# Kernel optimization log

Hardware: AMD Instinct MI355X
Metric: run time of the kernel (lower is better)

## Reference

```python
import jax, jax.numpy as jnp
import numpy as np

D_MODEL = 256

def setup_inputs() -> dict:
    key = jax.random.key(0)
    ks = jax.random.split(key, 6)
    B, Tx, Tm, D = 4, 512, 512, D_MODEL
    s = 1.0 / np.sqrt(D)
    return {
        "x": jax.random.normal(ks[0], (B, Tx, D), jnp.float32),
        "memory": jax.random.normal(ks[1], (B, Tm, D), jnp.float32),
        "memory_mask": jnp.ones((B, Tm), jnp.int32),
        "ws1_w": jax.random.uniform(ks[2], (D, D), jnp.float32, -s, s),
        "ws1_b": jax.random.uniform(ks[3], (D,), jnp.float32, -s, s),
        "ws2_w": jax.random.uniform(ks[4], (D, D), jnp.float32, -s, s),
        "wst_w": jax.random.uniform(ks[5], (D,), jnp.float32, -s, s),
    }

def reference(x, memory, memory_mask, ws1_w, ws1_b, ws2_w, wst_w):
    # item1: [B,Tx,D], item2: [B,Tm,D]  (torch Linear: y = x @ W^T + b)
    item1 = jnp.einsum("bxd,ed->bxe", x, ws1_w) + ws1_b
    item2 = jnp.einsum("bmd,ed->bme", memory, ws2_w)
    # broadcast add -> [B,Tx,Tm,D], tanh, reduce by wst -> scores [B,Tx,Tm]
    item = jnp.tanh(item1[:, :, None, :] + item2[:, None, :, :])
    S = jnp.einsum("bxmd,d->bxm", item, wst_w)
    S = jnp.where(memory_mask[:, None, :] == 0, -jnp.inf, S)
    S = jax.nn.softmax(S, axis=-1)
    out = jnp.einsum("bxm,bmd->bxd", S, memory)
    return (out, S)
```

## Files before the change

### kernel.cpp

```cpp
#include <hip/hip_runtime.h>

#define D_MODEL 256
#define TX 512
#define TM 512

__device__ __forceinline__ float fexp2(float x) { return __builtin_amdgcn_exp2f(x); }
__device__ __forceinline__ float frcp(float x)  { return __builtin_amdgcn_rcpf(x); }

__device__ __forceinline__ float quad(float4 a, float4 e, float4 w, float acc) {
    float p1 = fmaf(a.x, e.x, 1.f);
    float p2 = fmaf(a.y, e.y, 1.f);
    float p3 = fmaf(a.z, e.z, 1.f);
    float p4 = fmaf(a.w, e.w, 1.f);
    float p12 = p1 * p2;
    float p34 = p3 * p4;
    float q12 = fmaf(w.x, p2, w.y * p1);
    float q34 = fmaf(w.z, p4, w.w * p3);
    float N   = fmaf(q12, p34, q34 * p12);
    float D   = p12 * p34;
    return fmaf(N, frcp(D), acc);
}

__global__ __launch_bounds__(256) void gemm_exp2(
    const float* __restrict__ x,   const float* __restrict__ mem,
    const float* __restrict__ w1,  const float* __restrict__ b1,
    const float* __restrict__ w2,
    float* __restrict__ E1, float* __restrict__ E2p)
{
    const float C_SCALE = 2.8853900817779268f;
    const float* A; const float* W;
    int r0, n0;
    if (blockIdx.z == 0) { A = x;  W = w1; r0 = blockIdx.x * 64; n0 = blockIdx.y * 64; }
    else                 { A = w2; W = mem; r0 = blockIdx.y * 64; n0 = blockIdx.x * 64; }

    __shared__ float As[2][16][68];
    __shared__ float Ws[2][16][68];
    const int tid = threadIdx.x;
    const int tx = tid & 15, ty = tid >> 4;
    const int rl = tid >> 2, g = tid & 3;
    float acc[4][4] = {};
    const float* Ap = A + (size_t)(r0 + rl) * 256 + g * 4;
    const float* Wp = W + (size_t)(n0 + rl) * 256 + g * 4;

    {
        float4 a4 = *(const float4*)Ap;
        float4 w4 = *(const float4*)Wp;
        As[0][g*4+0][rl] = a4.x; As[0][g*4+1][rl] = a4.y;
        As[0][g*4+2][rl] = a4.z; As[0][g*4+3][rl] = a4.w;
        Ws[0][g*4+0][rl] = w4.x; Ws[0][g*4+1][rl] = w4.y;
        Ws[0][g*4+2][rl] = w4.z; Ws[0][g*4+3][rl] = w4.w;
    }
    __syncthreads();

    for (int k0 = 0; k0 < 16; ++k0) {
        const int cur = k0 & 1;
        float4 an, wn;
        if (k0 < 15) {
            an = *(const float4*)(Ap + (k0 + 1) * 16);
            wn = *(const float4*)(Wp + (k0 + 1) * 16);
        }
        #pragma unroll
        for (int kk = 0; kk < 16; ++kk) {
            float4 av = *(const float4*)&As[cur][kk][ty*4];
            float4 wv = *(const float4*)&Ws[cur][kk][tx*4];
            float a_[4] = {av.x, av.y, av.z, av.w};
            float w_[4] = {wv.x, wv.y, wv.z, wv.w};
            #pragma unroll
            for (int i = 0; i < 4; ++i)
                #pragma unroll
                for (int j = 0; j < 4; ++j)
                    acc[i][j] = fmaf(a_[i], w_[j], acc[i][j]);
        }
        if (k0 < 15) {
            const int nxt = cur ^ 1;
            As[nxt][g*4+0][rl] = an.x; As[nxt][g*4+1][rl] = an.y;
            As[nxt][g*4+2][rl] = an.z; As[nxt][g*4+3][rl] = an.w;
            Ws[nxt][g*4+0][rl] = wn.x; Ws[nxt][g*4+1][rl] = wn.y;
            Ws[nxt][g*4+2][rl] = wn.z; Ws[nxt][g*4+3][rl] = wn.w;
            __syncthreads();
        }
    }

    if (blockIdx.z == 0) {
        #pragma unroll
        for (int i = 0; i < 4; ++i) {
            const int r = r0 + ty*4 + i;
            #pragma unroll
            for (int j = 0; j < 4; ++j) {
                const int n = n0 + tx*4 + j;
                E1[(size_t)r*256 + n] = fexp2(C_SCALE * (acc[i][j] + b1[n]));
            }
        }
    } else {
        #pragma unroll
        for (int i = 0; i < 4; ++i) {
            const int r = r0 + ty*4 + i;
            #pragma unroll
            for (int j = 0; j < 4; ++j) {
                const int n = n0 + tx*4 + j;
                E2p[(size_t)(r >> 2)*8192 + (size_t)n*4 + (r & 3)] = fexp2(C_SCALE * acc[i][j]);
            }
        }
    }
}

__global__ __launch_bounds__(512) void fused_tanh_attn(
    const float* __restrict__ E1,
    const float* __restrict__ E2p,
    const float* __restrict__ memory,
    const int*   __restrict__ mask,
    const float* __restrict__ wst,
    float* __restrict__ out,
    float* __restrict__ Sout)
{
    const float LOG2E = 1.4426950408889634f;
    const int t = threadIdx.x;
    const int blk = (int)((blockIdx.x & 7) * 64 + (blockIdx.x >> 3));
    const int b = blk >> 7;
    const int x0 = (blk & 127) * 4;
    const int wave = t >> 6, lane = t & 63;
    const int tm = t & 255;
    const int dh = t >> 8;

    __shared__ float i1R[4][D_MODEL];
    __shared__ float wsh[D_MODEL];
    __shared__ float P[4][TM];
    __shared__ float mneg[TM];
    __shared__ float opart[8][4][D_MODEL];
    __shared__ float wpart[8];

    {
        const float* i1g = E1 + ((size_t)b * TX + x0) * D_MODEL;
        const int row = t >> 7, col2 = (t & 127) * 2;
        float2 v = *(const float2*)(i1g + (size_t)row * D_MODEL + col2);
        *(float2*)&i1R[row][col2] = v;
    }
    if (t < 256) wsh[t] = wst[t];
    mneg[t] = mask[b*TM + t] ? 0.f : -__builtin_inff();

    {
        float s = (t < 256) ? wst[t] : 0.f;
        #pragma unroll
        for (int off = 32; off > 0; off >>= 1) s += __shfl_xor(s, off);
        if (lane == 0) wpart[wave] = s;
    }

    const int g0 = dh * 32;
    const float* e2ptrA = E2p + ((size_t)b * TM + tm) * 4;
    const float* e2ptrB = e2ptrA + 1024;
    float4 e2a = *(const float4*)(e2ptrA + (size_t)g0 * 8192);
    float4 e2b = *(const float4*)(e2ptrB + (size_t)g0 * 8192);

    __syncthreads();
    const float Wsum = wpart[0] + wpart[1] + wpart[2] + wpart[3]
                     + wpart[4] + wpart[5] + wpart[6] + wpart[7];

    float accA[4] = {}, accB[4] = {};
    #pragma unroll 2
    for (int gi = 0; gi < 32; ++gi) {
        const int g = g0 + gi;
        float4 e2an = e2a, e2bn = e2b;
        if (gi < 31) {
            e2an = *(const float4*)(e2ptrA + (size_t)(g + 1) * 8192);
            e2bn = *(const float4*)(e2ptrB + (size_t)(g + 1) * 8192);
        }
        float4 w4 = *(const float4*)&wsh[g * 4];
        #pragma unroll
        for (int r = 0; r < 4; ++r) {
            float4 a = *(const float4*)&i1R[r][g * 4];
            accA[r] = quad(a, e2a, w4, accA[r]);
            accB[r] = quad(a, e2b, w4, accB[r]);
        }
        e2a = e2an; e2b = e2bn;
    }

    if (dh == 0) {
        #pragma unroll
        for (int r = 0; r < 4; ++r) {
            P[r][tm]       = accA[r];
            P[r][tm + 256] = accB[r];
        }
    }
    __syncthreads();
    if (dh == 1) {
        const float mnA = mneg[tm], mnB = mneg[tm + 256];
        #pragma unroll
        for (int r = 0; r < 4; ++r) {
            P[r][tm]       = Wsum - 2.f * (P[r][tm]       + accA[r]) + mnA;
            P[r][tm + 256] = Wsum - 2.f * (P[r][tm + 256] + accB[r]) + mnB;
        }
    }
    __syncthreads();

    if (wave < 4) {
        const int xx = wave;
        float4 u0 = *(const float4*)&P[xx][lane * 8];
        float4 u1 = *(const float4*)&P[xx][lane * 8 + 4];
        float v[8] = {u0.x,u0.y,u0.z,u0.w,u1.x,u1.y,u1.z,u1.w};
        float mx = v[0];
        #pragma unroll
        for (int q = 1; q < 8; ++q) mx = fmaxf(mx, v[q]);
        #pragma unroll
        for (int off = 32; off > 0; off >>= 1) mx = fmaxf(mx, __shfl_xor(mx, off));
        float e[8];
        float sum = 0.f;
        #pragma unroll
        for (int q = 0; q < 8; ++q) { e[q] = fexp2((v[q] - mx) * LOG2E); sum += e[q]; }
        #pragma unroll
        for (int off = 32; off > 0; off >>= 1) sum += __shfl_xor(sum, off);
        const float inv = frcp(sum);
        float4 p0 = {e[0]*inv, e[1]*inv, e[2]*inv, e[3]*inv};
        float4 p1 = {e[4]*inv, e[5]*inv, e[6]*inv, e[7]*inv};
        *(float4*)&P[xx][lane*8]   = p0;
        *(float4*)&P[xx][lane*8+4] = p1;
        float* Sg = Sout + ((size_t)b*TX + x0 + xx) * TM + lane*8;
        *(float4*)Sg     = p0;
        *(float4*)(Sg+4) = p1;
    }
    __syncthreads();

    {
        const int m0 = wave * 64;
        const float* memp = memory + ((size_t)b * TM + m0) * D_MODEL + lane * 4;
        float4 o0 = {0,0,0,0}, o1 = {0,0,0,0}, o2 = {0,0,0,0}, o3 = {0,0,0,0};
        for (int c = 0; c < 16; ++c) {
            float4 p0 = *(const float4*)&P[0][m0 + c*4];
            float4 p1 = *(const float4*)&P[1][m0 + c*4];
            float4 p2 = *(const float4*)&P[2][m0 + c*4];
            float4 p3 = *(const float4*)&P[3][m0 + c*4];
            #pragma unroll
            for (int j = 0; j < 4; ++j) {
                float4 mv = *(const float4*)(memp + (size_t)(c*4 + j) * D_MODEL);
                const float q0 = (j==0)?p0.x:(j==1)?p0.y:(j==2)?p0.z:p0.w;
                const float q1 = (j==0)?p1.x:(j==1)?p1.y:(j==2)?p1.z:p1.w;
                const float q2 = (j==0)?p2.x:(j==1)?p2.y:(j==2)?p2.z:p2.w;
                const float q3 = (j==0)?p3.x:(j==1)?p3.y:(j==2)?p3.z:p3.w;
                o0.x = fmaf(q0, mv.x, o0.x); o0.y = fmaf(q0, mv.y, o0.y);
                o0.z = fmaf(q0, mv.z, o0.z); o0.w = fmaf(q0, mv.w, o0.w);
                o1.x = fmaf(q1, mv.x, o1.x); o1.y = fmaf(q1, mv.y, o1.y);
                o1.z = fmaf(q1, mv.z, o1.z); o1.w = fmaf(q1, mv.w, o1.w);
                o2.x = fmaf(q2, mv.x, o2.x); o2.y = fmaf(q2, mv.y, o2.y);
                o2.z = fmaf(q2, mv.z, o2.z); o2.w = fmaf(q2, mv.w, o2.w);
                o3.x = fmaf(q3, mv.x, o3.x); o3.y = fmaf(q3, mv.y, o3.y);
                o3.z = fmaf(q3, mv.z, o3.z); o3.w = fmaf(q3, mv.w, o3.w);
            }
        }
        *(float4*)&opart[wave][0][lane*4] = o0;
        *(float4*)&opart[wave][1][lane*4] = o1;
        *(float4*)&opart[wave][2][lane*4] = o2;
        *(float4*)&opart[wave][3][lane*4] = o3;
    }
    __syncthreads();

    {
        #pragma unroll
        for (int k = 0; k < 2; ++k) {
            const int idx = t + k * 512;
            const int row = idx >> 8, d0 = idx & 255;
            float s = 0.f;
            #pragma unroll
            for (int w = 0; w < 8; ++w) s += opart[w][row][d0];
            out[((size_t)b*TX + x0 + row) * D_MODEL + d0] = s;
        }
    }
}

extern "C" void kernel_launch(void* const* d_in, const int* in_sizes, int n_in,
                              void* d_out, int out_size, void* d_ws, size_t ws_size,
                              hipStream_t stream) {
    const float* x    = (const float*)d_in[0];
    const float* mem  = (const float*)d_in[1];
    const int*   mask = (const int*)d_in[2];
    const float* w1   = (const float*)d_in[3];
    const float* b1   = (const float*)d_in[4];
    const float* w2   = (const float*)d_in[5];
    const float* wst  = (const float*)d_in[6];

    float* out  = (float*)d_out;
    float* Sout = out + 4 * 512 * 256;
    float* E1   = (float*)d_ws;
    float* E2p  = E1 + 4 * 512 * 256;

    dim3 gg(32, 4, 2);
    gemm_exp2<<<gg, 256, 0, stream>>>(x, mem, w1, b1, w2, E1, E2p);
    fused_tanh_attn<<<512, 512, 0, stream>>>(E1, E2p, mem, mask, wst, out, Sout);
}
```

Measured before the change: 56.43 us.

## Shrink GEMM tiles to 32x64, split softmax across all waves, prefetch memory rows

The GEMM prologue now uses 32x64 tiles with 128-thread blocks, doubling the block count from 256 to 512 for better CU occupancy, with the W tile loaded in two halves. In the attention kernel the two partial score halves go to separate shared arrays, and all 8 waves run the softmax with a two-way max/sum merge, where before 4 waves each handled a full row after an extra sync. The P·memory loop is fully unrolled with register double-buffering of memory rows to hide global load latency. The risks are more register pressure from the unroll and an extra barrier inside the softmax.

```diff
diff --git a/kernel.cpp b/kernel.cpp
--- a/kernel.cpp
+++ b/kernel.cpp
@@ -21,43 +21,49 @@
     return fmaf(N, frcp(D), acc);
 }
 
-__global__ __launch_bounds__(256) void gemm_exp2(
+__global__ __launch_bounds__(128) void gemm_exp2(
     const float* __restrict__ x,   const float* __restrict__ mem,
     const float* __restrict__ w1,  const float* __restrict__ b1,
     const float* __restrict__ w2,
     float* __restrict__ E1, float* __restrict__ E2p)
 {
     const float C_SCALE = 2.8853900817779268f;
+    const int bid = (int)blockIdx.x;
     const float* A; const float* W;
     int r0, n0;
-    if (blockIdx.z == 0) { A = x;  W = w1; r0 = blockIdx.x * 64; n0 = blockIdx.y * 64; }
-    else                 { A = w2; W = mem; r0 = blockIdx.y * 64; n0 = blockIdx.x * 64; }
-
-    __shared__ float As[2][16][68];
+    if (blockIdx.z == 0) { A = x;  W = w1; r0 = (bid & 63) * 32; n0 = (bid >> 6) * 64; }
+    else                 { A = w2; W = mem; r0 = (bid & 7) * 32;  n0 = (bid >> 3) * 64; }
+
+    __shared__ float As[2][16][36];
     __shared__ float Ws[2][16][68];
     const int tid = threadIdx.x;
     const int tx = tid & 15, ty = tid >> 4;
     const int rl = tid >> 2, g = tid & 3;
     float acc[4][4] = {};
-    const float* Ap = A + (size_t)(r0 + rl) * 256 + g * 4;
-    const float* Wp = W + (size_t)(n0 + rl) * 256 + g * 4;
+    const float* Ap  = A + (size_t)(r0 + rl) * 256 + g * 4;
+    const float* Wp0 = W + (size_t)(n0 + rl) * 256 + g * 4;
+    const float* Wp1 = W + (size_t)(n0 + 32 + rl) * 256 + g * 4;
 
     {
         float4 a4 = *(const float4*)Ap;
-        float4 w4 = *(const float4*)Wp;
+        float4 w4 = *(const float4*)Wp0;
+        float4 w5 = *(const float4*)Wp1;
         As[0][g*4+0][rl] = a4.x; As[0][g*4+1][rl] = a4.y;
         As[0][g*4+2][rl] = a4.z; As[0][g*4+3][rl] = a4.w;
         Ws[0][g*4+0][rl] = w4.x; Ws[0][g*4+1][rl] = w4.y;
         Ws[0][g*4+2][rl] = w4.z; Ws[0][g*4+3][rl] = w4.w;
+        Ws[0][g*4+0][rl+32] = w5.x; Ws[0][g*4+1][rl+32] = w5.y;
+        Ws[0][g*4+2][rl+32] = w5.z; Ws[0][g*4+3][rl+32] = w5.w;
     }
     __syncthreads();
 
     for (int k0 = 0; k0 < 16; ++k0) {
         const int cur = k0 & 1;
-        float4 an, wn;
+        float4 an, wn, vn;
         if (k0 < 15) {
-            an = *(const float4*)(Ap + (k0 + 1) * 16);
-            wn = *(const float4*)(Wp + (k0 + 1) * 16);
+            an = *(const float4*)(Ap  + (k0 + 1) * 16);
+            wn = *(const float4*)(Wp0 + (k0 + 1) * 16);
+            vn = *(const float4*)(Wp1 + (k0 + 1) * 16);
         }
         #pragma unroll
         for (int kk = 0; kk < 16; ++kk) {
@@ -77,6 +83,8 @@
             As[nxt][g*4+2][rl] = an.z; As[nxt][g*4+3][rl] = an.w;
             Ws[nxt][g*4+0][rl] = wn.x; Ws[nxt][g*4+1][rl] = wn.y;
             Ws[nxt][g*4+2][rl] = wn.z; Ws[nxt][g*4+3][rl] = wn.w;
+            Ws[nxt][g*4+0][rl+32] = vn.x; Ws[nxt][g*4+1][rl+32] = vn.y;
+            Ws[nxt][g*4+2][rl+32] = vn.z; Ws[nxt][g*4+3][rl+32] = vn.w;
             __syncthreads();
         }
     }
@@ -124,10 +132,12 @@
 
     __shared__ float i1R[4][D_MODEL];
     __shared__ float wsh[D_MODEL];
-    __shared__ float P[4][TM];
+    __shared__ float Pa[4][TM];
+    __shared__ float Pb[4][TM];
     __shared__ float mneg[TM];
     __shared__ float opart[8][4][D_MODEL];
     __shared__ float wpart[8];
+    __shared__ float smax[4][2], ssum[4][2];
 
     {
         const float* i1g = E1 + ((size_t)b * TX + x0) * D_MODEL;
@@ -176,46 +186,43 @@
 
     if (dh == 0) {
         #pragma unroll
-        for (int r = 0; r < 4; ++r) {
-            P[r][tm]       = accA[r];
-            P[r][tm + 256] = accB[r];
-        }
-    }
-    __syncthreads();
-    if (dh == 1) {
-        const float mnA = mneg[tm], mnB = mneg[tm + 256];
-        #pragma unroll
-        for (int r = 0; r < 4; ++r) {
-            P[r][tm]       = Wsum - 2.f * (P[r][tm]       + accA[r]) + mnA;
-            P[r][tm + 256] = Wsum - 2.f * (P[r][tm + 256] + accB[r]) + mnB;
-        }
-    }
-    __syncthreads();
-
-    if (wave < 4) {
-        const int xx = wave;
-        float4 u0 = *(const float4*)&P[xx][lane * 8];
-        float4 u1 = *(const float4*)&P[xx][lane * 8 + 4];
-        float v[8] = {u0.x,u0.y,u0.z,u0.w,u1.x,u1.y,u1.z,u1.w};
-        float mx = v[0];
-        #pragma unroll
-        for (int q = 1; q < 8; ++q) mx = fmaxf(mx, v[q]);
+        for (int r = 0; r < 4; ++r) { Pa[r][tm] = accA[r]; Pa[r][tm + 256] = accB[r]; }
+    } else {
+        #pragma unroll
+        for (int r = 0; r < 4; ++r) { Pb[r][tm] = accA[r]; Pb[r][tm + 256] = accB[r]; }
+    }
+    __syncthreads();
+
+    {
+        const int r = wave & 3, h = wave >> 2;
+        const int base = h * 256 + lane * 4;
+        float4 va = *(const float4*)&Pa[r][base];
+        float4 vb = *(const float4*)&Pb[r][base];
+        float4 mn = *(const float4*)&mneg[base];
+        float v0 = Wsum - 2.f * (va.x + vb.x) + mn.x;
+        float v1 = Wsum - 2.f * (va.y + vb.y) + mn.y;
+        float v2 = Wsum - 2.f * (va.z + vb.z) + mn.z;
+        float v3 = Wsum - 2.f * (va.w + vb.w) + mn.w;
+        float mx = fmaxf(fmaxf(v0, v1), fmaxf(v2, v3));
         #pragma unroll
         for (int off = 32; off > 0; off >>= 1) mx = fmaxf(mx, __shfl_xor(mx, off));
-        float e[8];
-        float sum = 0.f;
-        #pragma unroll
-        for (int q = 0; q < 8; ++q) { e[q] = fexp2((v[q] - mx) * LOG2E); sum += e[q]; }
+        float e0 = fexp2((v0 - mx) * LOG2E);
+        float e1 = fexp2((v1 - mx) * LOG2E);
+        float e2 = fexp2((v2 - mx) * LOG2E);
+        float e3 = fexp2((v3 - mx) * LOG2E);
+        float sum = (e0 + e1) + (e2 + e3);
         #pragma unroll
         for (int off = 32; off > 0; off >>= 1) sum += __shfl_xor(sum, off);
-        const float inv = frcp(sum);
-        float4 p0 = {e[0]*inv, e[1]*inv, e[2]*inv, e[3]*inv};
-        float4 p1 = {e[4]*inv, e[5]*inv, e[6]*inv, e[7]*inv};
-        *(float4*)&P[xx][lane*8]   = p0;
-        *(float4*)&P[xx][lane*8+4] = p1;
-        float* Sg = Sout + ((size_t)b*TX + x0 + xx) * TM + lane*8;
-        *(float4*)Sg     = p0;
-        *(float4*)(Sg+4) = p1;
+        if (lane == 0) { smax[r][h] = mx; ssum[r][h] = sum; }
+        __syncthreads();
+        const float m0 = smax[r][0], m1 = smax[r][1];
+        const float mg = fmaxf(m0, m1);
+        const float tot = ssum[r][0] * fexp2((m0 - mg) * LOG2E)
+                        + ssum[r][1] * fexp2((m1 - mg) * LOG2E);
+        const float fac = fexp2((mx - mg) * LOG2E) * frcp(tot);
+        float4 p = {e0 * fac, e1 * fac, e2 * fac, e3 * fac};
+        *(float4*)&Pa[r][base] = p;
+        *(float4*)(Sout + ((size_t)b*TX + x0 + r) * TM + base) = p;
     }
     __syncthreads();
 
@@ -223,14 +230,24 @@
         const int m0 = wave * 64;
         const float* memp = memory + ((size_t)b * TM + m0) * D_MODEL + lane * 4;
         float4 o0 = {0,0,0,0}, o1 = {0,0,0,0}, o2 = {0,0,0,0}, o3 = {0,0,0,0};
+        float4 mvA[4], mvB[4];
+        #pragma unroll
+        for (int j = 0; j < 4; ++j) mvA[j] = *(const float4*)(memp + (size_t)j * D_MODEL);
+        #pragma unroll
+        for (int j = 0; j < 4; ++j) mvB[j] = *(const float4*)(memp + (size_t)(4 + j) * D_MODEL);
+        #pragma unroll
         for (int c = 0; c < 16; ++c) {
-            float4 p0 = *(const float4*)&P[0][m0 + c*4];
-            float4 p1 = *(const float4*)&P[1][m0 + c*4];
-            float4 p2 = *(const float4*)&P[2][m0 + c*4];
-            float4 p3 = *(const float4*)&P[3][m0 + c*4];
+            float4 p0 = *(const float4*)&Pa[0][m0 + c*4];
+            float4 p1 = *(const float4*)&Pa[1][m0 + c*4];
+            float4 p2 = *(const float4*)&Pa[2][m0 + c*4];
+            float4 p3 = *(const float4*)&Pa[3][m0 + c*4];
             #pragma unroll
             for (int j = 0; j < 4; ++j) {
-                float4 mv = *(const float4*)(memp + (size_t)(c*4 + j) * D_MODEL);
+                float4 mv = (c & 1) ? mvB[j] : mvA[j];
+                if (c < 14) {
+                    float4 nf = *(const float4*)(memp + (size_t)((c + 2) * 4 + j) * D_MODEL);
+                    if (c & 1) mvB[j] = nf; else mvA[j] = nf;
+                }
                 const float q0 = (j==0)?p0.x:(j==1)?p0.y:(j==2)?p0.z:p0.w;
                 const float q1 = (j==0)?p1.x:(j==1)?p1.y:(j==2)?p1.z:p1.w;
                 const float q2 = (j==0)?p2.x:(j==1)?p2.y:(j==2)?p2.z:p2.w;
@@ -281,7 +298,7 @@
     float* E1   = (float*)d_ws;
     float* E2p  = E1 + 4 * 512 * 256;
 
-    dim3 gg(32, 4, 2);
-    gemm_exp2<<<gg, 256, 0, stream>>>(x, mem, w1, b1, w2, E1, E2p);
+    dim3 gg(256, 1, 2);
+    gemm_exp2<<<gg, 128, 0, stream>>>(x, mem, w1, b1, w2, E1, E2p);
     fused_tanh_attn<<<512, 512, 0, stream>>>(E1, E2p, mem, mask, wst, out, Sout);
 }
```

Result: slower. 64.61 us (+14.5%).
